# Optimization experiments

Measured on AMD Instinct MI355X. Metric: run time of the kernel, lower is better.

The kernel has to match this reference:

```python
import jax, jax.numpy as jnp
import numpy as np

B, T, C = 4, 2048, 2048
N, K = 16, 4          # query heads, kv heads
G, H = N // K, C // N # group size 4, head dim 128


def _rmsnorm(x):
    # RMSNorm over the full last (flattened N*H or K*H) axis, no scale param
    var = jnp.mean(jnp.square(x.astype(jnp.float32)), axis=-1, keepdims=True)
    return (x * jax.lax.rsqrt(var + 1e-06)).astype(x.dtype)


def _sine_table(features, length, max_timescale=10000.0):
    fraction = jnp.arange(0, features, 2, dtype=jnp.float32) / features
    timescale = max_timescale ** fraction
    sinusoid = jnp.einsum('i,j->ij', jnp.arange(length).astype(jnp.float32), 1.0 / timescale,
                          precision=jax.lax.Precision.HIGHEST)
    sinusoid = jnp.concatenate([sinusoid, sinusoid], axis=-1)  # [T, H]
    return jnp.sin(sinusoid), jnp.cos(sinusoid)


def _rotate_half(x):
    x1, x2 = jnp.split(x, 2, axis=-1)
    return jnp.concatenate([-x2, x1], axis=-1)


def setup_inputs() -> dict:
    key = jax.random.key(0)
    kx, kq, kk, kv, ko = jax.random.split(key, 5)
    q_std = float(np.sqrt(2.0 / (5.0 * C)))
    o_std = 2.0 / 24 / float(np.sqrt(N * H))  # wang init, n_layers=24
    return {
        'x': jax.random.normal(kx, (B, T, C), dtype=jnp.float32),
        'Wq': jax.random.normal(kq, (C, N * H), dtype=jnp.float32) * q_std,
        'Wk': jax.random.normal(kk, (C, K * H), dtype=jnp.float32) * q_std,
        'Wv': jax.random.normal(kv, (C, K * H), dtype=jnp.float32) * q_std,
        'Wout': jax.random.normal(ko, (N * H, C), dtype=jnp.float32) * o_std,
    }


def reference(x, Wq, Wk, Wv, Wout):
    b, t, c = x.shape
    q = _rmsnorm(x @ Wq)              # [B,T,N*H]
    k = _rmsnorm(x @ Wk)              # [B,T,K*H]
    v = x @ Wv                        # [B,T,K*H]
    q = q.reshape(b, t, K, G, H)
    k = k.reshape(b, t, K, H)
    v = v.reshape(b, t, K, H)

    sin, cos = _sine_table(H, t)      # [T,H]
    qcos, qsin = cos[None, :, None, None, :], sin[None, :, None, None, :]
    kcos, ksin = cos[None, :, None, :], sin[None, :, None, :]
    q = (q * qcos + _rotate_half(q) * qsin).astype(q.dtype)
    k = (k * kcos + _rotate_half(k) * ksin).astype(k.dtype)

    scale = jax.lax.rsqrt(jnp.array(H, dtype=jnp.float32)).astype(q.dtype)
    q = q * scale
    # full (non-causal) softmax attention; GQA: each kv head serves G query groups
    logits = jnp.einsum('btkgh,bskh->bkgts', q, k)
    probs = jax.nn.softmax(logits.astype(jnp.float32), axis=-1).astype(logits.dtype)
    enc = jnp.einsum('bkgts,bskh->btkgh', probs, v)  # [B,T,K,G,H]
    return enc.reshape(b, t, N * H) @ Wout
```

## Files before the change

kernel.cpp:

```cpp
#include <hip/hip_runtime.h>
#include <hip/hip_bf16.h>
#include <math.h>

typedef __attribute__((ext_vector_type(4))) float f32x4;
typedef __attribute__((ext_vector_type(8))) short s16x8;
typedef __attribute__((ext_vector_type(4))) short s16x4;

#define BB 4
#define TT 2048
#define CC 2048
#define NHEAD 16
#define KVH 4
#define HD 128
#define BT (BB*TT)
#define NHC 2048
#define KHC 512
#define QKVC 3072

__device__ __forceinline__ float bf2f(unsigned short u) {
  union { unsigned u; float f; } v; v.u = ((unsigned)u) << 16; return v.f;
}
__device__ __forceinline__ unsigned short f2bf(float f) {
  union { float f; unsigned u; } v; v.f = f;
  unsigned r = v.u + 0x7fff + ((v.u >> 16) & 1);
  return (unsigned short)(r >> 16);
}

#if defined(__has_builtin)
#if __has_builtin(__builtin_amdgcn_exp2f)
#define EXP2F(x) __builtin_amdgcn_exp2f(x)
#endif
#endif
#ifndef EXP2F
#define EXP2F(x) exp2f(x)
#endif

__device__ __forceinline__ void glld16(const void* gsrc, void* ldsbase) {
  __builtin_amdgcn_global_load_lds(
      (const __attribute__((address_space(1))) unsigned int*)gsrc,
      (__attribute__((address_space(3))) unsigned int*)(unsigned int)(unsigned long long)ldsbase,
      16, 0, 0);
}

__global__ void cvt_f2b(const float* __restrict__ in, unsigned short* __restrict__ out, int n4) {
  int i = blockIdx.x * 256 + threadIdx.x;
  if (i >= n4) return;
  float4 v = ((const float4*)in)[i];
  ushort4 o;
  o.x = f2bf(v.x); o.y = f2bf(v.y); o.z = f2bf(v.z); o.w = f2bf(v.w);
  ((ushort4*)out)[i] = o;
}

__global__ void trans_f2b(const float* __restrict__ in, unsigned short* __restrict__ out, int R, int Cc) {
  __shared__ float tile[32][33];
  int c0 = blockIdx.x * 32, r0 = blockIdx.y * 32;
  int tx = threadIdx.x, ty = threadIdx.y;
  #pragma unroll
  for (int k = 0; k < 4; k++)
    tile[ty + 8*k][tx] = in[(size_t)(r0 + ty + 8*k) * Cc + c0 + tx];
  __syncthreads();
  #pragma unroll
  for (int k = 0; k < 4; k++)
    out[(size_t)(c0 + ty + 8*k) * R + r0 + tx] = f2bf(tile[tx][ty + 8*k]);
}

__global__ void trans_v(const unsigned short* __restrict__ qkv, unsigned short* __restrict__ vT) {
  __shared__ unsigned short tile[32][33];
  int slice = blockIdx.z;
  int s0 = blockIdx.x * 32, h0 = blockIdx.y * 32;
  int tx = threadIdx.x, ty = threadIdx.y;
  const unsigned short* in = qkv + (size_t)(slice >> 2) * TT * QKVC + (NHC + KHC) + (slice & 3) * HD;
  unsigned short* out = vT + (size_t)slice * HD * TT;
  #pragma unroll
  for (int k = 0; k < 4; k++)
    tile[ty + 8*k][tx] = in[(size_t)(s0 + ty + 8*k) * QKVC + h0 + tx];
  __syncthreads();
  #pragma unroll
  for (int k = 0; k < 4; k++)
    out[(size_t)(h0 + ty + 8*k) * TT + s0 + tx] = tile[tx][ty + 8*k];
}

__global__ void sincos_init(float* __restrict__ stab, float* __restrict__ ctab) {
  int idx = blockIdx.x * 256 + threadIdx.x;
  if (idx >= TT * 64) return;
  int t = idx >> 6, i = idx & 63;
  double inv = exp(-log(10000.0) * ((double)i / 64.0));
  double ang = (double)t * inv;
  stab[idx] = (float)sin(ang);
  ctab[idx] = (float)cos(ang);
}

template<int OUTBF16>
__global__ __launch_bounds__(256) void gemm_nt(
    const unsigned short* __restrict__ A, const unsigned short* __restrict__ Bt,
    void* __restrict__ outp, int M, int Nn, int Kd) {
  __shared__ unsigned short As[128 * 32];
  __shared__ unsigned short Bs[128 * 32];
  int tid = threadIdx.x;
  int wave = tid >> 6, lane = tid & 63, q4 = lane >> 4, l16 = lane & 15;
  int m0 = blockIdx.y * 128, n0 = blockIdx.x * 128;
  int wm = (wave & 1) * 64, wn = (wave >> 1) * 64;
  f32x4 acc[4][4];
  #pragma unroll
  for (int i = 0; i < 4; i++)
    #pragma unroll
    for (int j = 0; j < 4; j++) acc[i][j] = f32x4{0.f, 0.f, 0.f, 0.f};

  int r0s = wave * 32 + (lane >> 2);
  int r1s = r0s + 16;
  int cg0 = (lane & 3) ^ ((r0s >> 1) & 3);
  int cg1 = (lane & 3) ^ ((r1s >> 1) & 3);
  const unsigned short* Ag0 = A + (size_t)(m0 + r0s) * Kd + cg0 * 8;
  const unsigned short* Ag1 = A + (size_t)(m0 + r1s) * Kd + cg1 * 8;
  const unsigned short* Bg0 = Bt + (size_t)(n0 + r0s) * Kd + cg0 * 8;
  const unsigned short* Bg1 = Bt + (size_t)(n0 + r1s) * Kd + cg1 * 8;
  unsigned short* lA0 = As + (wave * 2 + 0) * 512;
  unsigned short* lA1 = As + (wave * 2 + 1) * 512;
  unsigned short* lB0 = Bs + (wave * 2 + 0) * 512;
  unsigned short* lB1 = Bs + (wave * 2 + 1) * 512;

  int aoff[4], boff[4];
  #pragma unroll
  for (int f = 0; f < 4; f++) {
    int Ra = wm + f * 16 + l16;
    int Rb = wn + f * 16 + l16;
    aoff[f] = Ra * 32 + (q4 ^ ((Ra >> 1) & 3)) * 8;
    boff[f] = Rb * 32 + (q4 ^ ((Rb >> 1) & 3)) * 8;
  }

  for (int k0 = 0; k0 < Kd; k0 += 32) {
    __syncthreads();
    glld16(Ag0 + k0, lA0);
    glld16(Ag1 + k0, lA1);
    glld16(Bg0 + k0, lB0);
    glld16(Bg1 + k0, lB1);
    asm volatile("s_waitcnt vmcnt(0)" ::: "memory");
    __syncthreads();
    s16x8 af[4], bfr[4];
    #pragma unroll
    for (int mf = 0; mf < 4; mf++) af[mf] = *(const s16x8*)&As[aoff[mf]];
    #pragma unroll
    for (int nf = 0; nf < 4; nf++) bfr[nf] = *(const s16x8*)&Bs[boff[nf]];
    #pragma unroll
    for (int mf = 0; mf < 4; mf++)
      #pragma unroll
      for (int nf = 0; nf < 4; nf++)
        acc[mf][nf] = __builtin_amdgcn_mfma_f32_16x16x32_bf16(af[mf], bfr[nf], acc[mf][nf], 0, 0, 0);
  }
  #pragma unroll
  for (int mf = 0; mf < 4; mf++)
    #pragma unroll
    for (int nf = 0; nf < 4; nf++)
      #pragma unroll
      for (int r = 0; r < 4; r++) {
        int row = m0 + wm + mf*16 + q4*4 + r;
        int col = n0 + wn + nf*16 + l16;
        float v = acc[mf][nf][r];
        if (OUTBF16) ((unsigned short*)outp)[(size_t)row * Nn + col] = f2bf(v);
        else         ((float*)outp)[(size_t)row * Nn + col] = v;
      }
}

__global__ __launch_bounds__(256) void postproc(
    const unsigned short* __restrict__ qkv, unsigned short* __restrict__ qr,
    unsigned short* __restrict__ kr, const float* __restrict__ stab, const float* __restrict__ ctab) {
  __shared__ float sh[NHC + KHC];
  __shared__ float redq[4], redk[4];
  int row = blockIdx.x;
  int t = row & (TT - 1);
  int tid = threadIdx.x;
  const unsigned short* base = qkv + (size_t)row * QKVC;
  float sq = 0.f, sk = 0.f;
  uint4 qv = *(const uint4*)&base[tid * 8];
  const unsigned short* qp = (const unsigned short*)&qv;
  #pragma unroll
  for (int i = 0; i < 8; i++) { float f = bf2f(qp[i]); sh[tid*8 + i] = f; sq += f*f; }
  unsigned kv = *(const unsigned*)&base[NHC + tid*2];
  {
    float f0 = bf2f((unsigned short)(kv & 0xffff));
    float f1 = bf2f((unsigned short)(kv >> 16));
    sh[NHC + tid*2] = f0; sh[NHC + tid*2 + 1] = f1;
    sk += f0*f0 + f1*f1;
  }
  #pragma unroll
  for (int off = 32; off > 0; off >>= 1) { sq += __shfl_xor(sq, off); sk += __shfl_xor(sk, off); }
  if ((tid & 63) == 0) { redq[tid >> 6] = sq; redk[tid >> 6] = sk; }
  __syncthreads();
  float fq = rsqrtf((redq[0]+redq[1]+redq[2]+redq[3]) * (1.f/NHC) + 1e-6f)
             * (0.08838834764831845f * 1.4426950408889634f);
  float fk = rsqrtf((redk[0]+redk[1]+redk[2]+redk[3]) * (1.f/KHC) + 1e-6f);
  #pragma unroll
  for (int pi = 0; pi < 4; pi++) {
    int P = pi * 256 + tid;
    int head = P >> 6, i = P & 63;
    float s = stab[t*64 + i], c = ctab[t*64 + i];
    float x1 = sh[head*128 + i], x2 = sh[head*128 + i + 64];
    qr[(size_t)row * NHC + head*128 + i]      = f2bf((x1*c - x2*s) * fq);
    qr[(size_t)row * NHC + head*128 + i + 64] = f2bf((x2*c + x1*s) * fq);
  }
  {
    int head = tid >> 6, i = tid & 63;
    float s = stab[t*64 + i], c = ctab[t*64 + i];
    float x1 = sh[NHC + head*128 + i], x2 = sh[NHC + head*128 + i + 64];
    kr[(size_t)row * KHC + head*128 + i]      = f2bf((x1*c - x2*s) * fk);
    kr[(size_t)row * KHC + head*128 + i + 64] = f2bf((x2*c + x1*s) * fk);
  }
}

__global__ __launch_bounds__(256, 2) void attn(
    const unsigned short* __restrict__ qr, const unsigned short* __restrict__ kr,
    const unsigned short* __restrict__ vT, unsigned short* __restrict__ enc) {
  __shared__ unsigned short Ks[2][64 * 128];
  __shared__ unsigned short Vs[2][128 * 64];
  int tid = threadIdx.x;
  int wave = tid >> 6, lane = tid & 63, q4 = lane >> 4, l16 = lane & 15;
  int bid = blockIdx.x;
  int qt = bid & 15, n = (bid >> 4) & 15, b = bid >> 8, kh = n >> 2;

  const unsigned short* kbase = kr + ((size_t)(b * TT)) * KHC + kh * HD;
  const unsigned short* vbase = vT + ((size_t)((b * KVH + kh) * HD)) * TT;

  auto stageK = [&](int j, int kb) {
    const unsigned short* base = kbase + (size_t)(j * 64) * KHC;
    #pragma unroll
    for (int t = 0; t < 4; t++) {
      int L = wave * 4 + t;
      int r = L * 4 + (lane >> 4);
      int cg = (lane & 15) ^ (r & 7);
      glld16(base + (size_t)r * KHC + cg * 8, &Ks[kb][L * 512]);
    }
  };
  auto stageV = [&](int j, int vb) {
    const unsigned short* base = vbase + j * 64;
    #pragma unroll
    for (int t = 0; t < 4; t++) {
      int L = wave * 4 + t;
      int r = L * 8 + (lane >> 3);
      int cg = (lane & 7) ^ (r & 7);
      glld16(base + (size_t)r * TT + cg * 8, &Vs[vb][L * 512]);
    }
  };

  {
    const unsigned short* base = qr + ((size_t)(b * TT + qt * 128)) * NHC + n * HD;
    #pragma unroll
    for (int t = 0; t < 8; t++) {
      int L = wave * 8 + t;
      int r = L * 4 + (lane >> 4);
      int cg = (lane & 15) ^ (r & 7);
      glld16(base + (size_t)r * NHC + cg * 8, (unsigned short*)Ks + L * 512);
    }
  }
  stageV(0, 0);
  asm volatile("s_waitcnt vmcnt(0)" ::: "memory");
  __syncthreads();
  s16x8 qf[2][4];
  #pragma unroll
  for (int qb = 0; qb < 2; qb++)
    #pragma unroll
    for (int ku = 0; ku < 4; ku++) {
      int r = wave * 32 + qb * 16 + l16;
      qf[qb][ku] = *(const s16x8*)&((const unsigned short*)Ks)[r * 128 + (((ku * 4 + q4) ^ (r & 7)) << 3)];
    }
  __syncthreads();
  stageK(0, 0);
  asm volatile("s_waitcnt vmcnt(0)" ::: "memory");
  __syncthreads();

  float m_st[2] = {-1e30f, -1e30f}, l_st[2] = {0.f, 0.f};
  f32x4 O[2][8];
  #pragma unroll
  for (int qb = 0; qb < 2; qb++)
    #pragma unroll
    for (int hb = 0; hb < 8; hb++) O[qb][hb] = f32x4{0.f, 0.f, 0.f, 0.f};

  for (int j = 0; j < 32; j++) {
    int cur = j & 1;
    if (j < 31) { stageK(j + 1, cur ^ 1); stageV(j + 1, cur ^ 1); }
    f32x4 S[2][4];
    #pragma unroll
    for (int qb = 0; qb < 2; qb++)
      #pragma unroll
      for (int mb = 0; mb < 4; mb++) S[qb][mb] = f32x4{0.f, 0.f, 0.f, 0.f};
    __builtin_amdgcn_s_setprio(1);
    #pragma unroll
    for (int mb = 0; mb < 4; mb++) {
      int r = mb * 16 + l16;
      #pragma unroll
      for (int ku = 0; ku < 4; ku++) {
        s16x8 kf = *(const s16x8*)&Ks[cur][r * 128 + (((ku * 4 + q4) ^ (r & 7)) << 3)];
        S[0][mb] = __builtin_amdgcn_mfma_f32_16x16x32_bf16(kf, qf[0][ku], S[0][mb], 0, 0, 0);
        S[1][mb] = __builtin_amdgcn_mfma_f32_16x16x32_bf16(kf, qf[1][ku], S[1][mb], 0, 0, 0);
      }
    }
    __builtin_amdgcn_s_setprio(0);
    s16x8 pf8[2][2];
    #pragma unroll
    for (int qb = 0; qb < 2; qb++) {
      float mx = -1e30f;
      #pragma unroll
      for (int mb = 0; mb < 4; mb++)
        #pragma unroll
        for (int r = 0; r < 4; r++) mx = fmaxf(mx, S[qb][mb][r]);
      mx = fmaxf(mx, __shfl_xor(mx, 16));
      mx = fmaxf(mx, __shfl_xor(mx, 32));
      if (!__all(mx - m_st[qb] <= 8.f)) {
        float alpha = EXP2F(m_st[qb] - mx);
        m_st[qb] = mx;
        l_st[qb] *= alpha;
        #pragma unroll
        for (int hb = 0; hb < 8; hb++) O[qb][hb] *= alpha;
      }
      float mcur = m_st[qb];
      float rs = 0.f;
      #pragma unroll
      for (int mb = 0; mb < 4; mb++)
        #pragma unroll
        for (int r = 0; r < 4; r++) {
          float p = EXP2F(S[qb][mb][r] - mcur);
          rs += p;
          pf8[qb][mb >> 1][(mb & 1) * 4 + r] = (short)f2bf(p);
        }
      rs += __shfl_xor(rs, 16);
      rs += __shfl_xor(rs, 32);
      l_st[qb] += rs;
    }
    __builtin_amdgcn_s_setprio(1);
    #pragma unroll
    for (int su = 0; su < 2; su++) {
      #pragma unroll
      for (int hb = 0; hb < 8; hb++) {
        int r = hb * 16 + l16;
        int c0 = su * 8 + q4;
        int c1 = c0 + 4;
        s16x4 v0 = *(const s16x4*)&Vs[cur][r * 64 + (((c0 >> 1) ^ (r & 7)) << 3) + ((c0 & 1) << 2)];
        s16x4 v1 = *(const s16x4*)&Vs[cur][r * 64 + (((c1 >> 1) ^ (r & 7)) << 3) + ((c1 & 1) << 2)];
        s16x8 vf = __builtin_shufflevector(v0, v1, 0, 1, 2, 3, 4, 5, 6, 7);
        O[0][hb] = __builtin_amdgcn_mfma_f32_16x16x32_bf16(vf, pf8[0][su], O[0][hb], 0, 0, 0);
        O[1][hb] = __builtin_amdgcn_mfma_f32_16x16x32_bf16(vf, pf8[1][su], O[1][hb], 0, 0, 0);
      }
    }
    __builtin_amdgcn_s_setprio(0);
    asm volatile("s_waitcnt vmcnt(0)" ::: "memory");
    __syncthreads();
  }
  #pragma unroll
  for (int qb = 0; qb < 2; qb++) {
    float inv = 1.f / l_st[qb];
    int t = b * TT + qt * 128 + wave * 32 + qb * 16 + l16;
    #pragma unroll
    for (int hb = 0; hb < 8; hb++) {
      ushort4 o;
      o.x = f2bf(O[qb][hb][0] * inv);
      o.y = f2bf(O[qb][hb][1] * inv);
      o.z = f2bf(O[qb][hb][2] * inv);
      o.w = f2bf(O[qb][hb][3] * inv);
      *(ushort4*)&enc[(size_t)t * NHC + n * HD + hb * 16 + q4 * 4] = o;
    }
  }
}

extern "C" void kernel_launch(void* const* d_in, const int* in_sizes, int n_in,
                              void* d_out, int out_size, void* d_ws, size_t ws_size,
                              hipStream_t stream) {
  const float* x  = (const float*)d_in[0];
  const float* Wq = (const float*)d_in[1];
  const float* Wk = (const float*)d_in[2];
  const float* Wv = (const float*)d_in[3];
  const float* Wo = (const float*)d_in[4];
  float* out = (float*)d_out;

  char* ws = (char*)d_ws;
  size_t off = 0;
  auto alloc = [&](size_t bytes) -> void* {
    void* p = ws + off;
    off += (bytes + 255) & ~(size_t)255;
    return p;
  };
  unsigned short* xb    = (unsigned short*)alloc((size_t)BT * CC * 2);
  unsigned short* wqkvt = (unsigned short*)alloc((size_t)QKVC * CC * 2);
  unsigned short* wot   = (unsigned short*)alloc((size_t)CC * NHC * 2);
  unsigned short* qkv   = (unsigned short*)alloc((size_t)BT * QKVC * 2);
  unsigned short* qrb   = (unsigned short*)alloc((size_t)BT * NHC * 2);
  unsigned short* krb   = (unsigned short*)alloc((size_t)BT * KHC * 2);
  unsigned short* vTb   = (unsigned short*)alloc((size_t)BB * KVH * HD * TT * 2);
  unsigned short* encb  = (unsigned short*)alloc((size_t)BT * NHC * 2);
  float* stab = (float*)alloc((size_t)TT * 64 * 4);
  float* ctab = (float*)alloc((size_t)TT * 64 * 4);

  dim3 tb(32, 8);
  cvt_f2b<<<(BT*CC/4 + 255)/256, 256, 0, stream>>>(x, xb, BT*CC/4);
  trans_f2b<<<dim3(NHC/32, CC/32), tb, 0, stream>>>(Wq, wqkvt, CC, NHC);
  trans_f2b<<<dim3(KHC/32, CC/32), tb, 0, stream>>>(Wk, wqkvt + (size_t)NHC*CC, CC, KHC);
  trans_f2b<<<dim3(KHC/32, CC/32), tb, 0, stream>>>(Wv, wqkvt + (size_t)(NHC+KHC)*CC, CC, KHC);
  trans_f2b<<<dim3(NHC/32, NHC/32), tb, 0, stream>>>(Wo, wot, NHC, CC);
  sincos_init<<<(TT*64 + 255)/256, 256, 0, stream>>>(stab, ctab);
  gemm_nt<1><<<dim3(QKVC/128, BT/128), 256, 0, stream>>>(xb, wqkvt, qkv, BT, QKVC, CC);
  postproc<<<BT, 256, 0, stream>>>(qkv, qrb, krb, stab, ctab);
  trans_v<<<dim3(TT/32, HD/32, BB*KVH), tb, 0, stream>>>(qkv, vTb);
  attn<<<BB * NHEAD * (TT/128), 256, 0, stream>>>(qrb, krb, vTb, encb);
  gemm_nt<0><<<dim3(CC/128, BT/128), 256, 0, stream>>>(encb, wot, out, BT, CC, NHC);
}
```

Before: 559.8 us.

## Replace 128x128 GEMM with double-buffered 256x256 tile kernel and block swizzle

```diff
diff --git a/kernel.cpp b/kernel.cpp
--- a/kernel.cpp
+++ b/kernel.cpp
@@ -91,70 +91,88 @@
 }
 
 template<int OUTBF16>
-__global__ __launch_bounds__(256) void gemm_nt(
+__global__ __launch_bounds__(512, 2) void gemm256(
     const unsigned short* __restrict__ A, const unsigned short* __restrict__ Bt,
     void* __restrict__ outp, int M, int Nn, int Kd) {
-  __shared__ unsigned short As[128 * 32];
-  __shared__ unsigned short Bs[128 * 32];
+  __shared__ unsigned short As[2][256 * 64];
+  __shared__ unsigned short Bs[2][256 * 64];
   int tid = threadIdx.x;
   int wave = tid >> 6, lane = tid & 63, q4 = lane >> 4, l16 = lane & 15;
-  int m0 = blockIdx.y * 128, n0 = blockIdx.x * 128;
-  int wm = (wave & 1) * 64, wn = (wave >> 1) * 64;
-  f32x4 acc[4][4];
-  #pragma unroll
-  for (int i = 0; i < 4; i++)
+
+  int gx = Nn >> 8;
+  int nwg = gridDim.x;
+  int bid = blockIdx.x;
+  int bid2 = (nwg & 7) ? bid : ((bid & 7) * (nwg >> 3) + (bid >> 3));
+  int bx = bid2 % gx, by = bid2 / gx;
+  int m0 = by * 256, n0 = bx * 256;
+
+  int wm = (wave >> 2) * 128;
+  int wn = (wave & 3) * 64;
+
+  f32x4 acc[8][4];
+  #pragma unroll
+  for (int i = 0; i < 8; i++)
     #pragma unroll
     for (int j = 0; j < 4; j++) acc[i][j] = f32x4{0.f, 0.f, 0.f, 0.f};
 
-  int r0s = wave * 32 + (lane >> 2);
-  int r1s = r0s + 16;
-  int cg0 = (lane & 3) ^ ((r0s >> 1) & 3);
-  int cg1 = (lane & 3) ^ ((r1s >> 1) & 3);
-  const unsigned short* Ag0 = A + (size_t)(m0 + r0s) * Kd + cg0 * 8;
-  const unsigned short* Ag1 = A + (size_t)(m0 + r1s) * Kd + cg1 * 8;
-  const unsigned short* Bg0 = Bt + (size_t)(n0 + r0s) * Kd + cg0 * 8;
-  const unsigned short* Bg1 = Bt + (size_t)(n0 + r1s) * Kd + cg1 * 8;
-  unsigned short* lA0 = As + (wave * 2 + 0) * 512;
-  unsigned short* lA1 = As + (wave * 2 + 1) * 512;
-  unsigned short* lB0 = Bs + (wave * 2 + 0) * 512;
-  unsigned short* lB1 = Bs + (wave * 2 + 1) * 512;
-
-  int aoff[4], boff[4];
-  #pragma unroll
-  for (int f = 0; f < 4; f++) {
-    int Ra = wm + f * 16 + l16;
-    int Rb = wn + f * 16 + l16;
-    aoff[f] = Ra * 32 + (q4 ^ ((Ra >> 1) & 3)) * 8;
-    boff[f] = Rb * 32 + (q4 ^ ((Rb >> 1) & 3)) * 8;
-  }
-
-  for (int k0 = 0; k0 < Kd; k0 += 32) {
+  const unsigned short* Abase = A + (size_t)m0 * Kd;
+  const unsigned short* Bbase = Bt + (size_t)n0 * Kd;
+
+  auto stage = [&](const unsigned short* Ak, const unsigned short* Bk, int buf) {
+    #pragma unroll
+    for (int t = 0; t < 4; t++) {
+      int cf = (wave * 4 + t) * 64 + lane;
+      int r = cf >> 3, cg = (cf & 7) ^ (r & 7);
+      glld16(Ak + (size_t)r * Kd + cg * 8, &As[buf][(wave * 4 + t) * 512]);
+    }
+    #pragma unroll
+    for (int t = 0; t < 4; t++) {
+      int cf = (wave * 4 + t) * 64 + lane;
+      int r = cf >> 3, cg = (cf & 7) ^ (r & 7);
+      glld16(Bk + (size_t)r * Kd + cg * 8, &Bs[buf][(wave * 4 + t) * 512]);
+    }
+  };
+
+  stage(Abase, Bbase, 0);
+  __syncthreads();
+
+  int nkt = Kd >> 6;
+  for (int kt = 0; kt < nkt; kt++) {
+    int cur = kt & 1;
+    if (kt + 1 < nkt) stage(Abase + (kt + 1) * 64, Bbase + (kt + 1) * 64, cur ^ 1);
+    #pragma unroll
+    for (int ks = 0; ks < 2; ks++) {
+      s16x8 af[8], bfv[4];
+      int c = ks * 4 + q4;
+      #pragma unroll
+      for (int mf = 0; mf < 8; mf++) {
+        int r = wm + mf * 16 + l16;
+        af[mf] = *(const s16x8*)&As[cur][r * 64 + ((c ^ (r & 7)) << 3)];
+      }
+      #pragma unroll
+      for (int nf = 0; nf < 4; nf++) {
+        int r = wn + nf * 16 + l16;
+        bfv[nf] = *(const s16x8*)&Bs[cur][r * 64 + ((c ^ (r & 7)) << 3)];
+      }
+      __builtin_amdgcn_s_setprio(1);
+      #pragma unroll
+      for (int mf = 0; mf < 8; mf++)
+        #pragma unroll
+        for (int nf = 0; nf < 4; nf++)
+          acc[mf][nf] = __builtin_amdgcn_mfma_f32_16x16x32_bf16(af[mf], bfv[nf], acc[mf][nf], 0, 0, 0);
+      __builtin_amdgcn_s_setprio(0);
+    }
     __syncthreads();
-    glld16(Ag0 + k0, lA0);
-    glld16(Ag1 + k0, lA1);
-    glld16(Bg0 + k0, lB0);
-    glld16(Bg1 + k0, lB1);
-    asm volatile("s_waitcnt vmcnt(0)" ::: "memory");
-    __syncthreads();
-    s16x8 af[4], bfr[4];
-    #pragma unroll
-    for (int mf = 0; mf < 4; mf++) af[mf] = *(const s16x8*)&As[aoff[mf]];
-    #pragma unroll
-    for (int nf = 0; nf < 4; nf++) bfr[nf] = *(const s16x8*)&Bs[boff[nf]];
-    #pragma unroll
-    for (int mf = 0; mf < 4; mf++)
-      #pragma unroll
-      for (int nf = 0; nf < 4; nf++)
-        acc[mf][nf] = __builtin_amdgcn_mfma_f32_16x16x32_bf16(af[mf], bfr[nf], acc[mf][nf], 0, 0, 0);
-  }
-  #pragma unroll
-  for (int mf = 0; mf < 4; mf++)
+  }
+
+  #pragma unroll
+  for (int mf = 0; mf < 8; mf++)
     #pragma unroll
     for (int nf = 0; nf < 4; nf++)
       #pragma unroll
       for (int r = 0; r < 4; r++) {
-        int row = m0 + wm + mf*16 + q4*4 + r;
-        int col = n0 + wn + nf*16 + l16;
+        int row = m0 + wm + mf * 16 + q4 * 4 + r;
+        int col = n0 + wn + nf * 16 + l16;
         float v = acc[mf][nf][r];
         if (OUTBF16) ((unsigned short*)outp)[(size_t)row * Nn + col] = f2bf(v);
         else         ((float*)outp)[(size_t)row * Nn + col] = v;
@@ -395,9 +413,9 @@
   trans_f2b<<<dim3(KHC/32, CC/32), tb, 0, stream>>>(Wv, wqkvt + (size_t)(NHC+KHC)*CC, CC, KHC);
   trans_f2b<<<dim3(NHC/32, NHC/32), tb, 0, stream>>>(Wo, wot, NHC, CC);
   sincos_init<<<(TT*64 + 255)/256, 256, 0, stream>>>(stab, ctab);
-  gemm_nt<1><<<dim3(QKVC/128, BT/128), 256, 0, stream>>>(xb, wqkvt, qkv, BT, QKVC, CC);
+  gemm256<1><<<(BT/256) * (QKVC/256), 512, 0, stream>>>(xb, wqkvt, qkv, BT, QKVC, CC);
   postproc<<<BT, 256, 0, stream>>>(qkv, qrb, krb, stab, ctab);
   trans_v<<<dim3(TT/32, HD/32, BB*KVH), tb, 0, stream>>>(qkv, vTb);
   attn<<<BB * NHEAD * (TT/128), 256, 0, stream>>>(qrb, krb, vTb, encb);
-  gemm_nt<0><<<dim3(CC/128, BT/128), 256, 0, stream>>>(encb, wot, out, BT, CC, NHC);
-}
+  gemm256<0><<<(BT/256) * (CC/256), 512, 0, stream>>>(encb, wot, out, BT, CC, NHC);
+}
```

After: 525.4 us. -6.1%, faster.
